# Kernel tuning notes

Hardware: AMD Instinct MI355X
Metric: run time of the kernel (lower is better)

## Reference

```python
import jax, jax.numpy as jnp
import numpy as np

N_NODES = 100000
N_EDGES = 1600000
IN_CH = 128
OUT_CH = 64


def setup_inputs() -> dict:
    key = jax.random.key(0)
    k1, k2, k3 = jax.random.split(key, 3)
    x = jax.random.normal(k1, (N_NODES, IN_CH), dtype=jnp.float32)
    edge_index = jax.random.randint(k2, (2, N_EDGES), 0, N_NODES, dtype=jnp.int64)
    # Glorot-style init for the GCN weight, zero bias (PyG defaults)
    W = jax.random.normal(k3, (IN_CH, OUT_CH), dtype=jnp.float32) * (1.0 / np.sqrt(IN_CH))
    b = jnp.zeros((OUT_CH,), dtype=jnp.float32)
    return {"x": x, "edge_index": edge_index, "W": W, "b": b}


def reference(x, edge_index, W, b):
    n = x.shape[0]
    # add self loops (GCNConv default add_self_loops=True)
    loop = jnp.arange(n, dtype=edge_index.dtype)
    row = jnp.concatenate([edge_index[0], loop])  # source
    col = jnp.concatenate([edge_index[1], loop])  # target
    # symmetric degree normalization on augmented graph
    deg = jax.ops.segment_sum(jnp.ones_like(col, dtype=x.dtype), col, num_segments=n)
    dinv = jnp.where(deg > 0, jax.lax.rsqrt(deg), 0.0)
    norm = dinv[row] * dinv[col]  # [E+N]
    # linear transform first (out_channels < in_channels), then gather-scale-scatter
    h = x @ W  # [N, OUT]
    msgs = h[row] * norm[:, None]  # [E+N, OUT]
    out = jax.ops.segment_sum(msgs, col, num_segments=n)  # [N, OUT]
    return out + b
```

## Files before the change

### kernel.cpp

```cpp
#include <hip/hip_runtime.h>
#include <hip/hip_bf16.h>


#define IN_CH 128
#define OUT_CH 64
#define BSHIFT 7
#define BNODES 128
#define MAX_NB 800
#define CH_EDGES 8192
#define PSTRIDE 4096
#define SLOTS 32
#define SORT_CAP (BNODES * SLOTS)
#define OVSTRIDE 512
#define XSTR 136

typedef short bf16x8 __attribute__((ext_vector_type(8)));
typedef float f32x4  __attribute__((ext_vector_type(4)));

__device__ __forceinline__ unsigned short f2b(float f) {
    unsigned int u = __float_as_uint(f);
    return (unsigned short)((u + 0x7FFFu + ((u >> 16) & 1u)) >> 16);
}

__device__ __forceinline__ float blo(unsigned u) { return __uint_as_float(u << 16); }
__device__ __forceinline__ float bhi(unsigned u) { return __uint_as_float(u & 0xFFFF0000u); }

__global__ __launch_bounds__(256) void wprep_kernel(const float* __restrict__ W,
                                                    unsigned short* __restrict__ wbt,
                                                    int* __restrict__ cursor,
                                                    int NB) {
    int t = blockIdx.x * 256 + threadIdx.x;
    int k = t >> 6, nn = t & 63;
    wbt[nn * IN_CH + k] = f2b(W[t]);
    if (t < NB) cursor[t] = t * PSTRIDE;
}

__global__ __launch_bounds__(1024) void place_kernel(const int* __restrict__ row,
                                                     const int* __restrict__ col,
                                                     int* __restrict__ cursor,
                                                     int* __restrict__ pairs,
                                                     int E, int NB) {
    __shared__ int h[MAX_NB];
    int tid = threadIdx.x;
    for (int i = tid; i < NB; i += 1024) h[i] = 0;
    __syncthreads();
    int e0 = blockIdx.x * CH_EDGES;
    #pragma unroll
    for (int r1 = 0; r1 < CH_EDGES / 4096; ++r1) {
        int e = e0 + (r1 * 1024 + tid) * 4;
        if (e < E) {
            int4 c4 = *(const int4*)(col + e);
            atomicAdd(&h[c4.x >> BSHIFT], 1);
            atomicAdd(&h[c4.y >> BSHIFT], 1);
            atomicAdd(&h[c4.z >> BSHIFT], 1);
            atomicAdd(&h[c4.w >> BSHIFT], 1);
        }
    }
    __syncthreads();
    for (int i = tid; i < NB; i += 1024) {
        int c = h[i];
        if (c) h[i] = atomicAdd(&cursor[i], c);
    }
    __syncthreads();
    #pragma unroll
    for (int r2 = 0; r2 < CH_EDGES / 4096; ++r2) {
        int e = e0 + (r2 * 1024 + tid) * 4;
        if (e < E) {
            int4 c4 = *(const int4*)(col + e);
            int4 r4 = *(const int4*)(row + e);
            int b0 = c4.x >> BSHIFT, b1 = c4.y >> BSHIFT;
            int b2 = c4.z >> BSHIFT, b3 = c4.w >> BSHIFT;
            int p0 = atomicAdd(&h[b0], 1);
            pairs[p0] = r4.x | ((c4.x & (BNODES - 1)) << 17);
            int p1 = atomicAdd(&h[b1], 1);
            pairs[p1] = r4.y | ((c4.y & (BNODES - 1)) << 17);
            int p2 = atomicAdd(&h[b2], 1);
            pairs[p2] = r4.z | ((c4.z & (BNODES - 1)) << 17);
            int p3 = atomicAdd(&h[b3], 1);
            pairs[p3] = r4.w | ((c4.w & (BNODES - 1)) << 17);
        }
    }
}

__global__ __launch_bounds__(256) void bucket_sort_kernel(
    const int* __restrict__ cursor_end, const int* __restrict__ pairs,
    int* __restrict__ csr, int* __restrict__ ovpairs, int* __restrict__ ovcnt,
    unsigned char* __restrict__ degb, float* __restrict__ dinv, int n)
{
    __shared__ int cnt[BNODES];
    __shared__ int cur[BNODES];
    __shared__ __align__(16) int sorted[SORT_CAP];
    __shared__ int ovl[OVSTRIDE];
    __shared__ int ovc;

    int b = blockIdx.x, tid = threadIdx.x;
    int node0 = b << BSHIFT;
    int nodeCnt = min(BNODES, n - node0);
    int s0 = b * PSTRIDE;
    int m  = cursor_end[b] - s0;

    if (tid < BNODES) { cnt[tid] = 0; cur[tid] = 0; }
    if (tid == 0) ovc = 0;
    __syncthreads();
    for (int e = tid; e < m; e += 256) atomicAdd(&cnt[pairs[s0 + e] >> 17], 1);
    #pragma unroll
    for (int i = 0; i < SORT_CAP / 256; ++i) sorted[tid + i * 256] = n;
    __syncthreads();
    if (tid < nodeCnt) {
        int d = cnt[tid];
        degb[node0 + tid] = (unsigned char)min(d, 255);
        dinv[node0 + tid] = rsqrtf((float)(d + 1));
    }
    __syncthreads();
    for (int e = tid; e < m; e += 256) {
        int p   = pairs[s0 + e];
        int lc  = p >> 17;
        int pos = atomicAdd(&cur[lc], 1);
        if (pos < SLOTS) sorted[lc * SLOTS + pos] = p & 0x1FFFF;
        else {
            int o = atomicAdd(&ovc, 1);
            if (o < OVSTRIDE) ovl[o] = p;
        }
    }
    __syncthreads();
    {
        uint4* dst = (uint4*)(csr + node0 * SLOTS);
        const uint4* src = (const uint4*)sorted;
        #pragma unroll
        for (int i = 0; i < SORT_CAP / 1024; ++i)
            dst[tid + i * 256] = src[tid + i * 256];
    }
    int oc = min(ovc, OVSTRIDE);
    if (tid == 0) ovcnt[b] = oc;
    for (int i = tid; i < oc; i += 256) ovpairs[b * OVSTRIDE + i] = ovl[i];
}

__global__ __launch_bounds__(256) void gemm_kernel(
    const float* __restrict__ x, const unsigned short* __restrict__ wbt,
    const float* __restrict__ dinv, unsigned short* __restrict__ hpb, int n)
{
    __shared__ __align__(16) unsigned short xl[64 * XSTR];
    __shared__ __align__(16) unsigned short wl[64 * XSTR];

    int tid  = threadIdx.x;
    int row0 = blockIdx.x * 64;

    {
        const uint4* src = (const uint4*)wbt;
        #pragma unroll
        for (int i = 0; i < 4; ++i) {
            int flat = tid + i * 256;
            int nn = flat >> 4, c = flat & 15;
            *(uint4*)(wl + nn * XSTR + c * 8) = src[flat];
        }
    }
    #pragma unroll
    for (int i = 0; i < 4; ++i) {
        int r  = (tid >> 4) + i * 16;
        int c  = tid & 15;
        int gr = row0 + r;
        float4 v0 = make_float4(0.f,0.f,0.f,0.f), v1 = v0;
        float d = 0.f;
        if (gr < n) {
            d = dinv[gr];
            const float4* xr = (const float4*)(x + (size_t)gr * IN_CH);
            v0 = xr[c * 2]; v1 = xr[c * 2 + 1];
        }
        uint4 p;
        p.x = ((unsigned)f2b(v0.y * d) << 16) | f2b(v0.x * d);
        p.y = ((unsigned)f2b(v0.w * d) << 16) | f2b(v0.z * d);
        p.z = ((unsigned)f2b(v1.y * d) << 16) | f2b(v1.x * d);
        p.w = ((unsigned)f2b(v1.w * d) << 16) | f2b(v1.z * d);
        *(uint4*)(xl + r * XSTR + c * 8) = p;
    }
    __syncthreads();

    int lane = tid & 63, w = tid >> 6;
    int mrow = lane & 15;
    int g    = lane >> 4;

    f32x4 acc0 = {0,0,0,0}, acc1 = {0,0,0,0}, acc2 = {0,0,0,0}, acc3 = {0,0,0,0};
    const unsigned short* xbase = xl + (w * 16 + mrow) * XSTR + g * 8;
    const unsigned short* wbase = wl + mrow * XSTR + g * 8;

    #pragma unroll
    for (int k4 = 0; k4 < 4; ++k4) {
        bf16x8 a  = *(const bf16x8*)(xbase + k4 * 32);
        bf16x8 b0 = *(const bf16x8*)(wbase +             k4 * 32);
        bf16x8 b1 = *(const bf16x8*)(wbase + 16 * XSTR + k4 * 32);
        bf16x8 b2 = *(const bf16x8*)(wbase + 32 * XSTR + k4 * 32);
        bf16x8 b3 = *(const bf16x8*)(wbase + 48 * XSTR + k4 * 32);
        acc0 = __builtin_amdgcn_mfma_f32_16x16x32_bf16(a, b0, acc0, 0, 0, 0);
        acc1 = __builtin_amdgcn_mfma_f32_16x16x32_bf16(a, b1, acc1, 0, 0, 0);
        acc2 = __builtin_amdgcn_mfma_f32_16x16x32_bf16(a, b2, acc2, 0, 0, 0);
        acc3 = __builtin_amdgcn_mfma_f32_16x16x32_bf16(a, b3, acc3, 0, 0, 0);
    }
    __syncthreads();

    {
        int cm = g * 4;
        #pragma unroll
        for (int r = 0; r < 4; ++r) {
            unsigned short* crow = xl + (w * 16 + cm + r) * XSTR + mrow;
            crow[ 0] = f2b(acc0[r]);
            crow[16] = f2b(acc1[r]);
            crow[32] = f2b(acc2[r]);
            crow[48] = f2b(acc3[r]);
        }
    }
    __syncthreads();
    #pragma unroll
    for (int i = 0; i < 2; ++i) {
        int flat = tid + i * 256;
        int r = flat >> 3, c = flat & 7;
        int gr = row0 + r;
        if (gr <= n) {
            uint4 v = *(const uint4*)(xl + r * XSTR + c * 8);
            *(uint4*)(hpb + (size_t)gr * OUT_CH + c * 8) = v;
        }
    }
}

__global__ __launch_bounds__(256) void aggregate_kernel(
    const int* __restrict__ csr, const int* __restrict__ ovpairs,
    const int* __restrict__ ovcnt, const unsigned char* __restrict__ degb,
    const unsigned short* __restrict__ hpb, const float* __restrict__ dinv,
    const float* __restrict__ bias, float* __restrict__ out, int n)
{
    int wid  = (blockIdx.x * 256 + threadIdx.x) >> 6;
    int lane = threadIdx.x & 63;
    if (wid >= n) return;
    int e   = lane >> 3;
    int c   = lane & 7;
    int l31 = lane & 31;

    const uint4* hp16 = (const uint4*)hpb;

    int iv = csr[wid * SLOTS + l31];
    float d = dinv[wid];
    int deg = degb[wid];
    int bno = wid >> BSHIFT;
    int oc  = ovcnt[bno];
    uint4 sv = hp16[(unsigned)(wid * 8 + c)];

    int rnds = (min(deg, SLOTS) + 7) >> 3;

    float axl=0.f,axh=0.f, ayl=0.f,ayh=0.f, azl=0.f,azh=0.f, awl=0.f,awh=0.f;

    #define GATHER(SRC) \
        { int r_ = __shfl(iv, (SRC));                                            \
          uint4 v_ = hp16[(unsigned)(r_ * 8 + c)];                               \
          axl += blo(v_.x); axh += bhi(v_.x);                                    \
          ayl += blo(v_.y); ayh += bhi(v_.y);                                    \
          azl += blo(v_.z); azh += bhi(v_.z);                                    \
          awl += blo(v_.w); awh += bhi(v_.w); }

    if (rnds > 0) GATHER(     e)
    if (rnds > 1) GATHER( 8 + e)
    if (rnds > 2) GATHER(16 + e)
    if (rnds > 3) GATHER(24 + e)
    #undef GATHER

    if (oc > 0) {
        const int* op = ovpairs + bno * OVSTRIDE;
        for (int i = 0; i < oc; ++i) {
            int p    = op[i];
            int node = (bno << BSHIFT) + (p >> 17);
            if (node == wid) {
                uint4 v = hp16[(unsigned)((p & 0x1FFFF) * 8 + c)];
                if (e == 0) {
                    axl += blo(v.x); axh += bhi(v.x); ayl += blo(v.y); ayh += bhi(v.y);
                    azl += blo(v.z); azh += bhi(v.z); awl += blo(v.w); awh += bhi(v.w);
                }
            }
        }
    }

    #pragma unroll
    for (int m = 8; m < 64; m <<= 1) {
        axl += __shfl_xor(axl, m); axh += __shfl_xor(axh, m);
        ayl += __shfl_xor(ayl, m); ayh += __shfl_xor(ayh, m);
        azl += __shfl_xor(azl, m); azh += __shfl_xor(azh, m);
        awl += __shfl_xor(awl, m); awh += __shfl_xor(awh, m);
    }

    if (e == 0) {
        axl += blo(sv.x); axh += bhi(sv.x);
        ayl += blo(sv.y); ayh += bhi(sv.y);
        azl += blo(sv.z); azh += bhi(sv.z);
        awl += blo(sv.w); awh += bhi(sv.w);
        float4 b0 = ((const float4*)bias)[2 * c];
        float4 b1 = ((const float4*)bias)[2 * c + 1];
        float4 o0, o1;
        o0.x = fmaf(d, axl, b0.x); o0.y = fmaf(d, axh, b0.y);
        o0.z = fmaf(d, ayl, b0.z); o0.w = fmaf(d, ayh, b0.w);
        o1.x = fmaf(d, azl, b1.x); o1.y = fmaf(d, azh, b1.y);
        o1.z = fmaf(d, awl, b1.z); o1.w = fmaf(d, awh, b1.w);
        float* op = out + (size_t)wid * OUT_CH + c * 8;
        *(float4*)op       = o0;
        *(float4*)(op + 4) = o1;
    }
}

extern "C" void kernel_launch(void* const* d_in, const int* in_sizes, int n_in,
                              void* d_out, int out_size, void* d_ws, size_t ws_size,
                              hipStream_t stream) {
    const float* x  = (const float*)d_in[0];
    const int*   ei = (const int*)d_in[1];
    const float* W  = (const float*)d_in[2];
    const float* b  = (const float*)d_in[3];
    float*       out = (float*)d_out;

    int n = in_sizes[0] / IN_CH;
    int E = in_sizes[1] / 2;
    const int* row = ei;
    const int* col = ei + E;

    int NB   = (n + BNODES - 1) >> BSHIFT;
    int NBLK = (E + CH_EDGES - 1) / CH_EDGES;

    char* ws = (char*)d_ws;
    int*   cursor       = (int*)ws;   ws += (size_t)NB * 4;
    int*   ovcnt        = (int*)ws;   ws += (size_t)NB * 4;
    float* dinv         = (float*)ws; ws += (size_t)n * 4;
    unsigned char* degb = (unsigned char*)ws; ws += (size_t)(n + 2) & ~1ull; ws = (char*)(((uintptr_t)ws + 255) & ~(uintptr_t)255);
    unsigned short* wbt = (unsigned short*)ws; ws += (size_t)IN_CH * OUT_CH * 2;
    ws = (char*)(((uintptr_t)ws + 255) & ~(uintptr_t)255);
    int*   pairs        = (int*)ws;   ws += (size_t)NB * PSTRIDE * 4;
    int*   ovpairs      = (int*)ws;   ws += (size_t)NB * OVSTRIDE * 4;
    int*   csr          = (int*)ws;   ws += (size_t)NB * BNODES * SLOTS * 4;
    unsigned short* hpb = (unsigned short*)ws;

    wprep_kernel      <<<(IN_CH * OUT_CH) / 256, 256, 0, stream>>>(W, wbt, cursor, NB);
    place_kernel      <<<NBLK, 1024, 0, stream>>>(row, col, cursor, pairs, E, NB);
    bucket_sort_kernel<<<NB, 256, 0, stream>>>(cursor, pairs, csr, ovpairs, ovcnt, degb, dinv, n);
    gemm_kernel       <<<(n + 63) / 64, 256, 0, stream>>>(x, wbt, dinv, hpb, n);
    aggregate_kernel  <<<((size_t)n * 64 + 255) / 256, 256, 0, stream>>>(csr, ovpairs, ovcnt, degb, hpb, dinv, b, out, n);
}
```

Measured before the change: 170.8 us.

## Replace bucket-sort CSR build with direct per-node atomic slot placement

Drops the two-pass bucketed placement and the shared-memory bucket sort. Edges are now written straight into fixed 32-slot per-node CSR rows, using global atomics on per-node counters, and the rest go to a small global overflow list scanned with a ballot. Degree normalisation is computed inline from the node counters, so the dinv and degb arrays go away. This removes one kernel and the intermediate pairs buffer. In exchange it adds scattered global atomics and 4-byte scattered writes per edge, and overflow is now capped at 256 entries globally, which risks silently dropping edges on high-degree graphs.

```diff
diff --git a/kernel.cpp b/kernel.cpp
--- a/kernel.cpp
+++ b/kernel.cpp
@@ -4,14 +4,8 @@
 
 #define IN_CH 128
 #define OUT_CH 64
-#define BSHIFT 7
-#define BNODES 128
-#define MAX_NB 800
-#define CH_EDGES 8192
-#define PSTRIDE 4096
 #define SLOTS 32
-#define SORT_CAP (BNODES * SLOTS)
-#define OVSTRIDE 512
+#define OVCAP 256
 #define XSTR 136
 
 typedef short bf16x8 __attribute__((ext_vector_type(8)));
@@ -25,119 +19,46 @@
 __device__ __forceinline__ float blo(unsigned u) { return __uint_as_float(u << 16); }
 __device__ __forceinline__ float bhi(unsigned u) { return __uint_as_float(u & 0xFFFF0000u); }
 
-__global__ __launch_bounds__(256) void wprep_kernel(const float* __restrict__ W,
-                                                    unsigned short* __restrict__ wbt,
-                                                    int* __restrict__ cursor,
-                                                    int NB) {
+__global__ __launch_bounds__(256) void prep_kernel(const float* __restrict__ W,
+                                                   unsigned short* __restrict__ wbt,
+                                                   int* __restrict__ nodecnt,
+                                                   int4* __restrict__ csr4,
+                                                   int* __restrict__ ovc, int n) {
     int t = blockIdx.x * 256 + threadIdx.x;
-    int k = t >> 6, nn = t & 63;
-    wbt[nn * IN_CH + k] = f2b(W[t]);
-    if (t < NB) cursor[t] = t * PSTRIDE;
-}
-
-__global__ __launch_bounds__(1024) void place_kernel(const int* __restrict__ row,
+    if (t < n * 8) csr4[t] = make_int4(n, n, n, n);
+    if (t < IN_CH * OUT_CH) {
+        int k = t >> 6, nn = t & 63;
+        wbt[nn * IN_CH + k] = f2b(W[t]);
+    }
+    if (t < n) nodecnt[t] = 0;
+    if (t == 0) *ovc = 0;
+}
+
+__global__ __launch_bounds__(256) void place2_kernel(const int* __restrict__ row,
                                                      const int* __restrict__ col,
-                                                     int* __restrict__ cursor,
-                                                     int* __restrict__ pairs,
-                                                     int E, int NB) {
-    __shared__ int h[MAX_NB];
-    int tid = threadIdx.x;
-    for (int i = tid; i < NB; i += 1024) h[i] = 0;
-    __syncthreads();
-    int e0 = blockIdx.x * CH_EDGES;
-    #pragma unroll
-    for (int r1 = 0; r1 < CH_EDGES / 4096; ++r1) {
-        int e = e0 + (r1 * 1024 + tid) * 4;
-        if (e < E) {
-            int4 c4 = *(const int4*)(col + e);
-            atomicAdd(&h[c4.x >> BSHIFT], 1);
-            atomicAdd(&h[c4.y >> BSHIFT], 1);
-            atomicAdd(&h[c4.z >> BSHIFT], 1);
-            atomicAdd(&h[c4.w >> BSHIFT], 1);
-        }
-    }
-    __syncthreads();
-    for (int i = tid; i < NB; i += 1024) {
-        int c = h[i];
-        if (c) h[i] = atomicAdd(&cursor[i], c);
-    }
-    __syncthreads();
-    #pragma unroll
-    for (int r2 = 0; r2 < CH_EDGES / 4096; ++r2) {
-        int e = e0 + (r2 * 1024 + tid) * 4;
-        if (e < E) {
-            int4 c4 = *(const int4*)(col + e);
-            int4 r4 = *(const int4*)(row + e);
-            int b0 = c4.x >> BSHIFT, b1 = c4.y >> BSHIFT;
-            int b2 = c4.z >> BSHIFT, b3 = c4.w >> BSHIFT;
-            int p0 = atomicAdd(&h[b0], 1);
-            pairs[p0] = r4.x | ((c4.x & (BNODES - 1)) << 17);
-            int p1 = atomicAdd(&h[b1], 1);
-            pairs[p1] = r4.y | ((c4.y & (BNODES - 1)) << 17);
-            int p2 = atomicAdd(&h[b2], 1);
-            pairs[p2] = r4.z | ((c4.z & (BNODES - 1)) << 17);
-            int p3 = atomicAdd(&h[b3], 1);
-            pairs[p3] = r4.w | ((c4.w & (BNODES - 1)) << 17);
-        }
-    }
-}
-
-__global__ __launch_bounds__(256) void bucket_sort_kernel(
-    const int* __restrict__ cursor_end, const int* __restrict__ pairs,
-    int* __restrict__ csr, int* __restrict__ ovpairs, int* __restrict__ ovcnt,
-    unsigned char* __restrict__ degb, float* __restrict__ dinv, int n)
-{
-    __shared__ int cnt[BNODES];
-    __shared__ int cur[BNODES];
-    __shared__ __align__(16) int sorted[SORT_CAP];
-    __shared__ int ovl[OVSTRIDE];
-    __shared__ int ovc;
-
-    int b = blockIdx.x, tid = threadIdx.x;
-    int node0 = b << BSHIFT;
-    int nodeCnt = min(BNODES, n - node0);
-    int s0 = b * PSTRIDE;
-    int m  = cursor_end[b] - s0;
-
-    if (tid < BNODES) { cnt[tid] = 0; cur[tid] = 0; }
-    if (tid == 0) ovc = 0;
-    __syncthreads();
-    for (int e = tid; e < m; e += 256) atomicAdd(&cnt[pairs[s0 + e] >> 17], 1);
-    #pragma unroll
-    for (int i = 0; i < SORT_CAP / 256; ++i) sorted[tid + i * 256] = n;
-    __syncthreads();
-    if (tid < nodeCnt) {
-        int d = cnt[tid];
-        degb[node0 + tid] = (unsigned char)min(d, 255);
-        dinv[node0 + tid] = rsqrtf((float)(d + 1));
-    }
-    __syncthreads();
-    for (int e = tid; e < m; e += 256) {
-        int p   = pairs[s0 + e];
-        int lc  = p >> 17;
-        int pos = atomicAdd(&cur[lc], 1);
-        if (pos < SLOTS) sorted[lc * SLOTS + pos] = p & 0x1FFFF;
-        else {
-            int o = atomicAdd(&ovc, 1);
-            if (o < OVSTRIDE) ovl[o] = p;
-        }
-    }
-    __syncthreads();
-    {
-        uint4* dst = (uint4*)(csr + node0 * SLOTS);
-        const uint4* src = (const uint4*)sorted;
-        #pragma unroll
-        for (int i = 0; i < SORT_CAP / 1024; ++i)
-            dst[tid + i * 256] = src[tid + i * 256];
-    }
-    int oc = min(ovc, OVSTRIDE);
-    if (tid == 0) ovcnt[b] = oc;
-    for (int i = tid; i < oc; i += 256) ovpairs[b * OVSTRIDE + i] = ovl[i];
+                                                     int* __restrict__ nodecnt,
+                                                     int* __restrict__ csr,
+                                                     int* __restrict__ ovn,
+                                                     int* __restrict__ ovr,
+                                                     int* __restrict__ ovc, int E) {
+    int t = blockIdx.x * 256 + threadIdx.x;
+    int e = t * 4;
+    if (e >= E) return;
+    int4 c4 = *(const int4*)(col + e);
+    int4 r4 = *(const int4*)(row + e);
+    #define PUT(CN, RN)                                                   \
+        { int node = (CN), src = (RN);                                    \
+          int pos = atomicAdd(&nodecnt[node], 1);                         \
+          if (pos < SLOTS) csr[node * SLOTS + pos] = src;                 \
+          else { int o = atomicAdd(ovc, 1);                               \
+                 if (o < OVCAP) { ovn[o] = node; ovr[o] = src; } } }
+    PUT(c4.x, r4.x) PUT(c4.y, r4.y) PUT(c4.z, r4.z) PUT(c4.w, r4.w)
+    #undef PUT
 }
 
 __global__ __launch_bounds__(256) void gemm_kernel(
     const float* __restrict__ x, const unsigned short* __restrict__ wbt,
-    const float* __restrict__ dinv, unsigned short* __restrict__ hpb, int n)
+    const int* __restrict__ nodecnt, unsigned short* __restrict__ hpb, int n)
 {
     __shared__ __align__(16) unsigned short xl[64 * XSTR];
     __shared__ __align__(16) unsigned short wl[64 * XSTR];
@@ -162,7 +83,7 @@
         float4 v0 = make_float4(0.f,0.f,0.f,0.f), v1 = v0;
         float d = 0.f;
         if (gr < n) {
-            d = dinv[gr];
+            d = rsqrtf((float)(nodecnt[gr] + 1));
             const float4* xr = (const float4*)(x + (size_t)gr * IN_CH);
             v0 = xr[c * 2]; v1 = xr[c * 2 + 1];
         }
@@ -222,9 +143,10 @@
 }
 
 __global__ __launch_bounds__(256) void aggregate_kernel(
-    const int* __restrict__ csr, const int* __restrict__ ovpairs,
-    const int* __restrict__ ovcnt, const unsigned char* __restrict__ degb,
-    const unsigned short* __restrict__ hpb, const float* __restrict__ dinv,
+    const int* __restrict__ csr, const int* __restrict__ nodecnt,
+    const int* __restrict__ ovn, const int* __restrict__ ovr,
+    const int* __restrict__ ovc,
+    const unsigned short* __restrict__ hpb,
     const float* __restrict__ bias, float* __restrict__ out, int n)
 {
     int wid  = (blockIdx.x * 256 + threadIdx.x) >> 6;
@@ -236,14 +158,13 @@
 
     const uint4* hp16 = (const uint4*)hpb;
 
-    int iv = csr[wid * SLOTS + l31];
-    float d = dinv[wid];
-    int deg = degb[wid];
-    int bno = wid >> BSHIFT;
-    int oc  = ovcnt[bno];
+    int iv  = csr[wid * SLOTS + l31];
+    int dg  = nodecnt[wid];
+    int oc  = *ovc;
     uint4 sv = hp16[(unsigned)(wid * 8 + c)];
 
-    int rnds = (min(deg, SLOTS) + 7) >> 3;
+    float d = rsqrtf((float)(dg + 1));
+    int rnds = (min(dg, SLOTS) + 7) >> 3;
 
     float axl=0.f,axh=0.f, ayl=0.f,ayh=0.f, azl=0.f,azh=0.f, awl=0.f,awh=0.f;
 
@@ -262,15 +183,22 @@
     #undef GATHER
 
     if (oc > 0) {
-        const int* op = ovpairs + bno * OVSTRIDE;
-        for (int i = 0; i < oc; ++i) {
-            int p    = op[i];
-            int node = (bno << BSHIFT) + (p >> 17);
-            if (node == wid) {
-                uint4 v = hp16[(unsigned)((p & 0x1FFFF) * 8 + c)];
+        oc = min(oc, OVCAP);
+        for (int base = 0; base < oc; base += 64) {
+            int i  = base + lane;
+            int nd = (i < oc) ? ovn[i] : -1;
+            int rs = (i < oc) ? ovr[i] : 0;
+            unsigned long long mm = __ballot(nd == wid);
+            while (mm) {
+                int bit = __ffsll((long long)mm) - 1;
+                mm &= mm - 1;
+                int r_ = __shfl(rs, base == 0 ? bit : bit);
+                uint4 v_ = hp16[(unsigned)(r_ * 8 + c)];
                 if (e == 0) {
-                    axl += blo(v.x); axh += bhi(v.x); ayl += blo(v.y); ayh += bhi(v.y);
-                    azl += blo(v.z); azh += bhi(v.z); awl += blo(v.w); awh += bhi(v.w);
+                    axl += blo(v_.x); axh += bhi(v_.x);
+                    ayl += blo(v_.y); ayh += bhi(v_.y);
+                    azl += blo(v_.z); azh += bhi(v_.z);
+                    awl += blo(v_.w); awh += bhi(v_.w);
                 }
             }
         }
@@ -316,24 +244,22 @@
     const int* row = ei;
     const int* col = ei + E;
 
-    int NB   = (n + BNODES - 1) >> BSHIFT;
-    int NBLK = (E + CH_EDGES - 1) / CH_EDGES;
-
     char* ws = (char*)d_ws;
-    int*   cursor       = (int*)ws;   ws += (size_t)NB * 4;
-    int*   ovcnt        = (int*)ws;   ws += (size_t)NB * 4;
-    float* dinv         = (float*)ws; ws += (size_t)n * 4;
-    unsigned char* degb = (unsigned char*)ws; ws += (size_t)(n + 2) & ~1ull; ws = (char*)(((uintptr_t)ws + 255) & ~(uintptr_t)255);
+    int*   nodecnt = (int*)ws;  ws += (size_t)n * 4;
+    int*   ovc     = (int*)ws;  ws += 256;
+    int*   ovn     = (int*)ws;  ws += (size_t)OVCAP * 4;
+    int*   ovr     = (int*)ws;  ws += (size_t)OVCAP * 4;
     unsigned short* wbt = (unsigned short*)ws; ws += (size_t)IN_CH * OUT_CH * 2;
     ws = (char*)(((uintptr_t)ws + 255) & ~(uintptr_t)255);
-    int*   pairs        = (int*)ws;   ws += (size_t)NB * PSTRIDE * 4;
-    int*   ovpairs      = (int*)ws;   ws += (size_t)NB * OVSTRIDE * 4;
-    int*   csr          = (int*)ws;   ws += (size_t)NB * BNODES * SLOTS * 4;
+    int*   csr     = (int*)ws;  ws += (size_t)n * SLOTS * 4;
+    ws = (char*)(((uintptr_t)ws + 255) & ~(uintptr_t)255);
     unsigned short* hpb = (unsigned short*)ws;
 
-    wprep_kernel      <<<(IN_CH * OUT_CH) / 256, 256, 0, stream>>>(W, wbt, cursor, NB);
-    place_kernel      <<<NBLK, 1024, 0, stream>>>(row, col, cursor, pairs, E, NB);
-    bucket_sort_kernel<<<NB, 256, 0, stream>>>(cursor, pairs, csr, ovpairs, ovcnt, degb, dinv, n);
-    gemm_kernel       <<<(n + 63) / 64, 256, 0, stream>>>(x, wbt, dinv, hpb, n);
-    aggregate_kernel  <<<((size_t)n * 64 + 255) / 256, 256, 0, stream>>>(csr, ovpairs, ovcnt, degb, hpb, dinv, b, out, n);
-}
+    int prep_blk   = (n * 8 + 255) / 256;
+    int place_blk  = (E / 4 + 255) / 256;
+
+    prep_kernel     <<<prep_blk, 256, 0, stream>>>(W, wbt, nodecnt, (int4*)csr, ovc, n);
+    place2_kernel   <<<place_blk, 256, 0, stream>>>(row, col, nodecnt, csr, ovn, ovr, ovc, E);
+    gemm_kernel     <<<(n + 63) / 64, 256, 0, stream>>>(x, wbt, nodecnt, hpb, n);
+    aggregate_kernel<<<((size_t)n * 64 + 255) / 256, 256, 0, stream>>>(csr, nodecnt, ovn, ovr, ovc, hpb, b, out, n);
+}
```

Result: slower. 276.5 us (+61.9%).

## Fuse bucket sort into aggregation and compute degrees via global atomics in place

Applied to the files above, without the earlier changes.

Drops the separate bucket-sort kernel and the global CSR/overflow buffers. Each block now sorts its bucket's pairs in shared memory and immediately aggregates its 128 nodes. Per-node degrees come from global atomic counters updated in the place kernel, so the GEMM can compute dinv directly. This removes a launch and the round trip of CSR data through global memory. In exchange it adds 1.6M global atomics, cuts aggregation parallelism to one block of 8 waves per 128 nodes, and halves the overflow capacity.

```diff
diff --git a/kernel.cpp b/kernel.cpp
--- a/kernel.cpp
+++ b/kernel.cpp
@@ -11,7 +11,7 @@
 #define PSTRIDE 4096
 #define SLOTS 32
 #define SORT_CAP (BNODES * SLOTS)
-#define OVSTRIDE 512
+#define OVB 256
 #define XSTR 136
 
 typedef short bf16x8 __attribute__((ext_vector_type(8)));
@@ -25,19 +25,24 @@
 __device__ __forceinline__ float blo(unsigned u) { return __uint_as_float(u << 16); }
 __device__ __forceinline__ float bhi(unsigned u) { return __uint_as_float(u & 0xFFFF0000u); }
 
-__global__ __launch_bounds__(256) void wprep_kernel(const float* __restrict__ W,
-                                                    unsigned short* __restrict__ wbt,
-                                                    int* __restrict__ cursor,
-                                                    int NB) {
+__global__ __launch_bounds__(256) void prep_kernel(const float* __restrict__ W,
+                                                   unsigned short* __restrict__ wbt,
+                                                   int* __restrict__ cursor,
+                                                   int* __restrict__ nodecnt,
+                                                   int NB, int n) {
     int t = blockIdx.x * 256 + threadIdx.x;
-    int k = t >> 6, nn = t & 63;
-    wbt[nn * IN_CH + k] = f2b(W[t]);
+    if (t < IN_CH * OUT_CH) {
+        int k = t >> 6, nn = t & 63;
+        wbt[nn * IN_CH + k] = f2b(W[t]);
+    }
     if (t < NB) cursor[t] = t * PSTRIDE;
+    if (t < n) nodecnt[t] = 0;
 }
 
 __global__ __launch_bounds__(1024) void place_kernel(const int* __restrict__ row,
                                                      const int* __restrict__ col,
                                                      int* __restrict__ cursor,
+                                                     int* __restrict__ nodecnt,
                                                      int* __restrict__ pairs,
                                                      int E, int NB) {
     __shared__ int h[MAX_NB];
@@ -54,6 +59,10 @@
             atomicAdd(&h[c4.y >> BSHIFT], 1);
             atomicAdd(&h[c4.z >> BSHIFT], 1);
             atomicAdd(&h[c4.w >> BSHIFT], 1);
+            atomicAdd(&nodecnt[c4.x], 1);
+            atomicAdd(&nodecnt[c4.y], 1);
+            atomicAdd(&nodecnt[c4.z], 1);
+            atomicAdd(&nodecnt[c4.w], 1);
         }
     }
     __syncthreads();
@@ -68,76 +77,21 @@
         if (e < E) {
             int4 c4 = *(const int4*)(col + e);
             int4 r4 = *(const int4*)(row + e);
-            int b0 = c4.x >> BSHIFT, b1 = c4.y >> BSHIFT;
-            int b2 = c4.z >> BSHIFT, b3 = c4.w >> BSHIFT;
-            int p0 = atomicAdd(&h[b0], 1);
+            int p0 = atomicAdd(&h[c4.x >> BSHIFT], 1);
             pairs[p0] = r4.x | ((c4.x & (BNODES - 1)) << 17);
-            int p1 = atomicAdd(&h[b1], 1);
+            int p1 = atomicAdd(&h[c4.y >> BSHIFT], 1);
             pairs[p1] = r4.y | ((c4.y & (BNODES - 1)) << 17);
-            int p2 = atomicAdd(&h[b2], 1);
+            int p2 = atomicAdd(&h[c4.z >> BSHIFT], 1);
             pairs[p2] = r4.z | ((c4.z & (BNODES - 1)) << 17);
-            int p3 = atomicAdd(&h[b3], 1);
+            int p3 = atomicAdd(&h[c4.w >> BSHIFT], 1);
             pairs[p3] = r4.w | ((c4.w & (BNODES - 1)) << 17);
         }
     }
-}
-
-__global__ __launch_bounds__(256) void bucket_sort_kernel(
-    const int* __restrict__ cursor_end, const int* __restrict__ pairs,
-    int* __restrict__ csr, int* __restrict__ ovpairs, int* __restrict__ ovcnt,
-    unsigned char* __restrict__ degb, float* __restrict__ dinv, int n)
-{
-    __shared__ int cnt[BNODES];
-    __shared__ int cur[BNODES];
-    __shared__ __align__(16) int sorted[SORT_CAP];
-    __shared__ int ovl[OVSTRIDE];
-    __shared__ int ovc;
-
-    int b = blockIdx.x, tid = threadIdx.x;
-    int node0 = b << BSHIFT;
-    int nodeCnt = min(BNODES, n - node0);
-    int s0 = b * PSTRIDE;
-    int m  = cursor_end[b] - s0;
-
-    if (tid < BNODES) { cnt[tid] = 0; cur[tid] = 0; }
-    if (tid == 0) ovc = 0;
-    __syncthreads();
-    for (int e = tid; e < m; e += 256) atomicAdd(&cnt[pairs[s0 + e] >> 17], 1);
-    #pragma unroll
-    for (int i = 0; i < SORT_CAP / 256; ++i) sorted[tid + i * 256] = n;
-    __syncthreads();
-    if (tid < nodeCnt) {
-        int d = cnt[tid];
-        degb[node0 + tid] = (unsigned char)min(d, 255);
-        dinv[node0 + tid] = rsqrtf((float)(d + 1));
-    }
-    __syncthreads();
-    for (int e = tid; e < m; e += 256) {
-        int p   = pairs[s0 + e];
-        int lc  = p >> 17;
-        int pos = atomicAdd(&cur[lc], 1);
-        if (pos < SLOTS) sorted[lc * SLOTS + pos] = p & 0x1FFFF;
-        else {
-            int o = atomicAdd(&ovc, 1);
-            if (o < OVSTRIDE) ovl[o] = p;
-        }
-    }
-    __syncthreads();
-    {
-        uint4* dst = (uint4*)(csr + node0 * SLOTS);
-        const uint4* src = (const uint4*)sorted;
-        #pragma unroll
-        for (int i = 0; i < SORT_CAP / 1024; ++i)
-            dst[tid + i * 256] = src[tid + i * 256];
-    }
-    int oc = min(ovc, OVSTRIDE);
-    if (tid == 0) ovcnt[b] = oc;
-    for (int i = tid; i < oc; i += 256) ovpairs[b * OVSTRIDE + i] = ovl[i];
 }
 
 __global__ __launch_bounds__(256) void gemm_kernel(
     const float* __restrict__ x, const unsigned short* __restrict__ wbt,
-    const float* __restrict__ dinv, unsigned short* __restrict__ hpb, int n)
+    const int* __restrict__ nodecnt, unsigned short* __restrict__ hpb, int n)
 {
     __shared__ __align__(16) unsigned short xl[64 * XSTR];
     __shared__ __align__(16) unsigned short wl[64 * XSTR];
@@ -162,7 +116,7 @@
         float4 v0 = make_float4(0.f,0.f,0.f,0.f), v1 = v0;
         float d = 0.f;
         if (gr < n) {
-            d = dinv[gr];
+            d = rsqrtf((float)(nodecnt[gr] + 1));
             const float4* xr = (const float4*)(x + (size_t)gr * IN_CH);
             v0 = xr[c * 2]; v1 = xr[c * 2 + 1];
         }
@@ -221,84 +175,113 @@
     }
 }
 
-__global__ __launch_bounds__(256) void aggregate_kernel(
-    const int* __restrict__ csr, const int* __restrict__ ovpairs,
-    const int* __restrict__ ovcnt, const unsigned char* __restrict__ degb,
-    const unsigned short* __restrict__ hpb, const float* __restrict__ dinv,
+__global__ __launch_bounds__(512) void sortagg_kernel(
+    const int* __restrict__ cursor_end, const int* __restrict__ pairs,
+    const unsigned short* __restrict__ hpb,
     const float* __restrict__ bias, float* __restrict__ out, int n)
 {
-    int wid  = (blockIdx.x * 256 + threadIdx.x) >> 6;
-    int lane = threadIdx.x & 63;
-    if (wid >= n) return;
-    int e   = lane >> 3;
-    int c   = lane & 7;
-    int l31 = lane & 31;
-
+    __shared__ int cnt[BNODES];
+    __shared__ int cur[BNODES];
+    __shared__ __align__(16) int sorted[SORT_CAP];
+    __shared__ int ovl[OVB];
+    __shared__ int ovc;
+
+    int b = blockIdx.x, tid = threadIdx.x;
+    int node0 = b << BSHIFT;
+    int nodeCnt = min(BNODES, n - node0);
+    int s0 = b * PSTRIDE;
+    int m  = cursor_end[b] - s0;
+
+    if (tid < BNODES) { cnt[tid] = 0; cur[tid] = 0; }
+    if (tid == 0) ovc = 0;
+    #pragma unroll
+    for (int i = 0; i < SORT_CAP / 512; ++i) sorted[tid + i * 512] = n;
+    __syncthreads();
+    for (int e = tid; e < m; e += 512) atomicAdd(&cnt[pairs[s0 + e] >> 17], 1);
+    __syncthreads();
+    for (int e = tid; e < m; e += 512) {
+        int p   = pairs[s0 + e];
+        int lc  = p >> 17;
+        int pos = atomicAdd(&cur[lc], 1);
+        if (pos < SLOTS) sorted[lc * SLOTS + pos] = p & 0x1FFFF;
+        else {
+            int o = atomicAdd(&ovc, 1);
+            if (o < OVB) ovl[o] = p;
+        }
+    }
+    __syncthreads();
+    int oc = min(ovc, OVB);
+
+    int lane = tid & 63, w = tid >> 6;
+    int e = lane >> 3, c = lane & 7, l31 = lane & 31;
     const uint4* hp16 = (const uint4*)hpb;
 
-    int iv = csr[wid * SLOTS + l31];
-    float d = dinv[wid];
-    int deg = degb[wid];
-    int bno = wid >> BSHIFT;
-    int oc  = ovcnt[bno];
-    uint4 sv = hp16[(unsigned)(wid * 8 + c)];
-
-    int rnds = (min(deg, SLOTS) + 7) >> 3;
-
-    float axl=0.f,axh=0.f, ayl=0.f,ayh=0.f, azl=0.f,azh=0.f, awl=0.f,awh=0.f;
-
-    #define GATHER(SRC) \
-        { int r_ = __shfl(iv, (SRC));                                            \
-          uint4 v_ = hp16[(unsigned)(r_ * 8 + c)];                               \
-          axl += blo(v_.x); axh += bhi(v_.x);                                    \
-          ayl += blo(v_.y); ayh += bhi(v_.y);                                    \
-          azl += blo(v_.z); azh += bhi(v_.z);                                    \
-          awl += blo(v_.w); awh += bhi(v_.w); }
-
-    if (rnds > 0) GATHER(     e)
-    if (rnds > 1) GATHER( 8 + e)
-    if (rnds > 2) GATHER(16 + e)
-    if (rnds > 3) GATHER(24 + e)
-    #undef GATHER
-
-    if (oc > 0) {
-        const int* op = ovpairs + bno * OVSTRIDE;
-        for (int i = 0; i < oc; ++i) {
-            int p    = op[i];
-            int node = (bno << BSHIFT) + (p >> 17);
-            if (node == wid) {
-                uint4 v = hp16[(unsigned)((p & 0x1FFFF) * 8 + c)];
-                if (e == 0) {
-                    axl += blo(v.x); axh += bhi(v.x); ayl += blo(v.y); ayh += bhi(v.y);
-                    azl += blo(v.z); azh += bhi(v.z); awl += blo(v.w); awh += bhi(v.w);
+    for (int ii = 0; ii < BNODES / 8; ++ii) {
+        int i = w * (BNODES / 8) + ii;
+        if (i >= nodeCnt) break;
+        int node = node0 + i;
+
+        int iv = sorted[i * SLOTS + l31];
+        int dg = cnt[i];
+        uint4 sv = hp16[(unsigned)(node * 8 + c)];
+        float d = rsqrtf((float)(dg + 1));
+        int rnds = (min(dg, SLOTS) + 7) >> 3;
+
+        float axl=0.f,axh=0.f, ayl=0.f,ayh=0.f, azl=0.f,azh=0.f, awl=0.f,awh=0.f;
+
+        #define GATHER(SRC) \
+            { int r_ = __shfl(iv, (SRC));                                        \
+              uint4 v_ = hp16[(unsigned)(r_ * 8 + c)];                           \
+              axl += blo(v_.x); axh += bhi(v_.x);                                \
+              ayl += blo(v_.y); ayh += bhi(v_.y);                                \
+              azl += blo(v_.z); azh += bhi(v_.z);                                \
+              awl += blo(v_.w); awh += bhi(v_.w); }
+
+        if (rnds > 0) GATHER(     e)
+        if (rnds > 1) GATHER( 8 + e)
+        if (rnds > 2) GATHER(16 + e)
+        if (rnds > 3) GATHER(24 + e)
+        #undef GATHER
+
+        if (oc > 0) {
+            for (int o = 0; o < oc; ++o) {
+                int p = ovl[o];
+                if ((p >> 17) == i) {
+                    uint4 v_ = hp16[(unsigned)((p & 0x1FFFF) * 8 + c)];
+                    if (e == 0) {
+                        axl += blo(v_.x); axh += bhi(v_.x);
+                        ayl += blo(v_.y); ayh += bhi(v_.y);
+                        azl += blo(v_.z); azh += bhi(v_.z);
+                        awl += blo(v_.w); awh += bhi(v_.w);
+                    }
                 }
             }
         }
-    }
-
-    #pragma unroll
-    for (int m = 8; m < 64; m <<= 1) {
-        axl += __shfl_xor(axl, m); axh += __shfl_xor(axh, m);
-        ayl += __shfl_xor(ayl, m); ayh += __shfl_xor(ayh, m);
-        azl += __shfl_xor(azl, m); azh += __shfl_xor(azh, m);
-        awl += __shfl_xor(awl, m); awh += __shfl_xor(awh, m);
-    }
-
-    if (e == 0) {
-        axl += blo(sv.x); axh += bhi(sv.x);
-        ayl += blo(sv.y); ayh += bhi(sv.y);
-        azl += blo(sv.z); azh += bhi(sv.z);
-        awl += blo(sv.w); awh += bhi(sv.w);
-        float4 b0 = ((const float4*)bias)[2 * c];
-        float4 b1 = ((const float4*)bias)[2 * c + 1];
-        float4 o0, o1;
-        o0.x = fmaf(d, axl, b0.x); o0.y = fmaf(d, axh, b0.y);
-        o0.z = fmaf(d, ayl, b0.z); o0.w = fmaf(d, ayh, b0.w);
-        o1.x = fmaf(d, azl, b1.x); o1.y = fmaf(d, azh, b1.y);
-        o1.z = fmaf(d, awl, b1.z); o1.w = fmaf(d, awh, b1.w);
-        float* op = out + (size_t)wid * OUT_CH + c * 8;
-        *(float4*)op       = o0;
-        *(float4*)(op + 4) = o1;
+
+        #pragma unroll
+        for (int mm = 8; mm < 64; mm <<= 1) {
+            axl += __shfl_xor(axl, mm); axh += __shfl_xor(axh, mm);
+            ayl += __shfl_xor(ayl, mm); ayh += __shfl_xor(ayh, mm);
+            azl += __shfl_xor(azl, mm); azh += __shfl_xor(azh, mm);
+            awl += __shfl_xor(awl, mm); awh += __shfl_xor(awh, mm);
+        }
+
+        if (e == 0) {
+            axl += blo(sv.x); axh += bhi(sv.x);
+            ayl += blo(sv.y); ayh += bhi(sv.y);
+            azl += blo(sv.z); azh += bhi(sv.z);
+            awl += blo(sv.w); awh += bhi(sv.w);
+            float4 b0 = ((const float4*)bias)[2 * c];
+            float4 b1 = ((const float4*)bias)[2 * c + 1];
+            float4 o0, o1;
+            o0.x = fmaf(d, axl, b0.x); o0.y = fmaf(d, axh, b0.y);
+            o0.z = fmaf(d, ayl, b0.z); o0.w = fmaf(d, ayh, b0.w);
+            o1.x = fmaf(d, azl, b1.x); o1.y = fmaf(d, azh, b1.y);
+            o1.z = fmaf(d, awl, b1.z); o1.w = fmaf(d, awh, b1.w);
+            float* op = out + (size_t)node * OUT_CH + c * 8;
+            *(float4*)op       = o0;
+            *(float4*)(op + 4) = o1;
+        }
     }
 }
 
@@ -320,20 +303,16 @@
     int NBLK = (E + CH_EDGES - 1) / CH_EDGES;
 
     char* ws = (char*)d_ws;
-    int*   cursor       = (int*)ws;   ws += (size_t)NB * 4;
-    int*   ovcnt        = (int*)ws;   ws += (size_t)NB * 4;
-    float* dinv         = (float*)ws; ws += (size_t)n * 4;
-    unsigned char* degb = (unsigned char*)ws; ws += (size_t)(n + 2) & ~1ull; ws = (char*)(((uintptr_t)ws + 255) & ~(uintptr_t)255);
+    int*   cursor  = (int*)ws;  ws += (size_t)NB * 4;
+    int*   nodecnt = (int*)ws;  ws += (size_t)n * 4;
     unsigned short* wbt = (unsigned short*)ws; ws += (size_t)IN_CH * OUT_CH * 2;
     ws = (char*)(((uintptr_t)ws + 255) & ~(uintptr_t)255);
-    int*   pairs        = (int*)ws;   ws += (size_t)NB * PSTRIDE * 4;
-    int*   ovpairs      = (int*)ws;   ws += (size_t)NB * OVSTRIDE * 4;
-    int*   csr          = (int*)ws;   ws += (size_t)NB * BNODES * SLOTS * 4;
+    int*   pairs   = (int*)ws;  ws += (size_t)NB * PSTRIDE * 4;
+    ws = (char*)(((uintptr_t)ws + 255) & ~(uintptr_t)255);
     unsigned short* hpb = (unsigned short*)ws;
 
-    wprep_kernel      <<<(IN_CH * OUT_CH) / 256, 256, 0, stream>>>(W, wbt, cursor, NB);
-    place_kernel      <<<NBLK, 1024, 0, stream>>>(row, col, cursor, pairs, E, NB);
-    bucket_sort_kernel<<<NB, 256, 0, stream>>>(cursor, pairs, csr, ovpairs, ovcnt, degb, dinv, n);
-    gemm_kernel       <<<(n + 63) / 64, 256, 0, stream>>>(x, wbt, dinv, hpb, n);
-    aggregate_kernel  <<<((size_t)n * 64 + 255) / 256, 256, 0, stream>>>(csr, ovpairs, ovcnt, degb, hpb, dinv, b, out, n);
-}
+    prep_kernel   <<<(n + 255) / 256, 256, 0, stream>>>(W, wbt, cursor, nodecnt, NB, n);
+    place_kernel  <<<NBLK, 1024, 0, stream>>>(row, col, cursor, nodecnt, pairs, E, NB);
+    gemm_kernel   <<<(n + 63) / 64, 256, 0, stream>>>(x, wbt, nodecnt, hpb, n);
+    sortagg_kernel<<<NB, 512, 0, stream>>>(cursor, pairs, hpb, b, out, n);
+}
```

Measured after the change: 232.8 us. 36.3% more time.
